# Performance work log

Measured on AMD Instinct MI355X. Metric: run time of the kernel, lower is better.

## Reference

```python
import jax, jax.numpy as jnp
import numpy as np

DN = ('NCHW', 'OIHW', 'NCHW')  # conv dimension numbers
EPS = 1e-5


def _tcn(x, w1, b1, w2, b2, w3, b3):
    """Gated TCN. x: [B,T,N,C] -> [B,T-2,N,Cout].  out = conv1(x)*sigmoid(conv2(x)) + tanh(conv3(x))"""
    xc = jnp.transpose(x, (0, 3, 2, 1))  # [B,C,N,T]
    conv = lambda w, b: jax.lax.conv_general_dilated(xc, w, (1, 1), 'VALID', dimension_numbers=DN) + b[None, :, None, None]
    p = conv(w1, b1)
    q = jax.nn.sigmoid(conv(w2, b2))
    r = jnp.tanh(conv(w3, b3))
    out = p * q + r  # [B,Cout,N,T-2]
    return jnp.transpose(out, (0, 3, 2, 1))


def setup_inputs() -> dict:
    key = jax.random.key(0)
    ks = jax.random.split(key, 16)
    B, T, N, C_in = 32, 24, 1024, 1
    K, C_t, C_s = 3, 64, 16
    inp = {}
    inp['x'] = jax.random.normal(ks[0], (B, T, N, C_in), jnp.float32)
    # stacked Chebyshev polynomials T_0..T_{K-1}, scaled so matmul output stays O(1)
    inp['cheb'] = jax.random.normal(ks[1], (K, N, N), jnp.float32) * (N ** -0.5)
    # temporal conv 1 (C_in -> C_t), kernel (1,3)
    s1 = (2.0 / (C_in * 3 + C_t * 3)) ** 0.5
    for i, nm in enumerate(['t1_w1', 't1_w2', 't1_w3']):
        inp[nm] = jax.random.normal(ks[2 + i], (C_t, C_in, 1, 3), jnp.float32) * s1
        inp[nm.replace('w', 'b')] = jnp.zeros((C_t,), jnp.float32)
    # Chebyshev weights (K, C_t, C_s), xavier-normal
    sc = (2.0 / (C_t + C_s)) ** 0.5
    inp['w_cheb'] = jax.random.normal(ks[5], (K, C_t, C_s), jnp.float32) * sc
    inp['b_cheb'] = jnp.zeros((C_s,), jnp.float32)
    # temporal conv 2 (C_s -> C_s)
    s2 = (2.0 / (C_s * 3 + C_s * 3)) ** 0.5
    for i, nm in enumerate(['t2_w1', 't2_w2', 't2_w3']):
        inp[nm] = jax.random.normal(ks[6 + i], (C_s, C_s, 1, 3), jnp.float32) * s2
        inp[nm.replace('w', 'b')] = jnp.zeros((C_s,), jnp.float32)
    # BatchNorm2d over num_nodes channel
    inp['bn_gamma'] = jnp.ones((N,), jnp.float32)
    inp['bn_beta'] = jnp.zeros((N,), jnp.float32)
    return inp


def reference(x, cheb, t1_w1, t1_b1, t1_w2, t1_b2, t1_w3, t1_b3,
              w_cheb, b_cheb, t2_w1, t2_b1, t2_w2, t2_b2, t2_w3, t2_b3,
              bn_gamma, bn_beta):
    # gated TCN 1: [B,24,N,1] -> [B,22,N,64]
    h = _tcn(x, t1_w1, t1_b1, t1_w2, t1_b2, t1_w3, t1_b3)
    # Chebyshev graph conv fused over all time steps and K taps:
    # T_k_x[b,t,n,c] = sum_m h[b,t,m,c] * cheb[k,m,n]; out = sum_k T_k_x @ W[k]
    s = jnp.einsum('btmc,kmn,kco->btno', h, cheb, w_cheb) + b_cheb  # [B,22,N,16]
    # gated TCN 2: -> [B,20,N,16]
    h2 = _tcn(s, t2_w1, t2_b1, t2_w2, t2_b2, t2_w3, t2_b3)
    # BatchNorm2d over node dim (training-mode batch stats), matching permute(0,2,1,3)
    y = jnp.transpose(h2, (0, 2, 1, 3))  # [B,N,T',C]
    mean = jnp.mean(y, axis=(0, 2, 3), keepdims=True)
    var = jnp.var(y, axis=(0, 2, 3), keepdims=True)  # biased, like torch BN
    y = (y - mean) * jax.lax.rsqrt(var + EPS) * bn_gamma[None, :, None, None] + bn_beta[None, :, None, None]
    y = jnp.transpose(y, (0, 2, 1, 3))  # [B,T',N,C]
    return jax.nn.relu(y)
```

## Files before the change

kernel.cpp:

```cpp
#include <hip/hip_runtime.h>
#include <hip/hip_bf16.h>

using bf16x8 = __attribute__((ext_vector_type(8))) short;
using bf16x4 = __attribute__((ext_vector_type(4))) short;
using f32x4  = __attribute__((ext_vector_type(4))) float;
using f32x2  = __attribute__((ext_vector_type(2))) float;

static __device__ __forceinline__ float bf2f(short s) {
  union { unsigned u; float f; } z;
  z.u = ((unsigned)(unsigned short)s) << 16;
  return z.f;
}
static __device__ __forceinline__ short f2bfs(float f) {
  union { __hip_bfloat16 h; short s; } u;
  u.h = __float2bfloat16(f);
  return u.s;
}
static __device__ __forceinline__ float frcp(float x) { return __builtin_amdgcn_rcpf(x); }
static __device__ __forceinline__ float sigm_f(float x) { return frcp(1.f + __expf(-x)); }
static __device__ __forceinline__ float tanh_f(float x) {
  return fmaf(2.f, frcp(1.f + __expf(-2.f * x)), -1.f);
}

typedef const __attribute__((address_space(1))) unsigned int* gas_u32;
typedef __attribute__((address_space(3))) unsigned int* las_u32;
#define GLOAD16(gp, lp) __builtin_amdgcn_global_load_lds( \
    (gas_u32)(const void*)(gp), (las_u32)(void*)(lp), 16, 0, 0)

__global__ void __launch_bounds__(256) k_transpose_cheb(
    const float* __restrict__ cheb, __hip_bfloat16* __restrict__ chebT,
    const float* __restrict__ wcheb, __hip_bfloat16* __restrict__ pbw) {
  int blk = blockIdx.x;
  if (blk == 768) {
    for (int i = threadIdx.x; i < 3072; i += 256) {
      int jj = i & 7, lane = (i >> 3) & 63, ksk = i >> 9;
      int kk = ksk >> 1, ks = ksk & 1;
      int c = ks * 32 + ((lane >> 4) & 3) * 8 + jj;
      int o = lane & 15;
      pbw[i] = __float2bfloat16(wcheb[kk * 1024 + c * 16 + o]);
    }
    return;
  }
  __shared__ float tile[64][65];
  int k = blk >> 8;
  int rem = blk & 255;
  int m0 = (rem >> 4) << 6;
  int n0 = (rem & 15) << 6;
  int tx = threadIdx.x & 63;
  int ty = threadIdx.x >> 6;
  const float* src = cheb + (size_t)k * 1024 * 1024;
  #pragma unroll
  for (int i = 0; i < 16; i++) {
    int ml = ty + i * 4;
    tile[ml][tx] = src[(size_t)(m0 + ml) * 1024 + n0 + tx];
  }
  __syncthreads();
  #pragma unroll
  for (int i = 0; i < 16; i++) {
    int nl = ty + i * 4;
    chebT[(size_t)(n0 + nl) * 3072 + k * 1024 + m0 + tx] =
        __float2bfloat16(tile[tx][nl]);
  }
}

__global__ void __launch_bounds__(256) k_tcn1_proj(
    const float* __restrict__ x,
    const float* __restrict__ w1, const float* __restrict__ b1,
    const float* __restrict__ w2, const float* __restrict__ b2,
    const float* __restrict__ w3, const float* __restrict__ b3,
    const __hip_bfloat16* __restrict__ pbw,
    __hip_bfloat16* __restrict__ hwt, int bt0) {
  __shared__ __align__(16) char hls[32768];
  const int tid = threadIdx.x;
  const int lane = tid & 63, w = tid >> 6;
  const int r16 = lane & 15, kb = lane >> 4;
  const int btl = blockIdx.x >> 2;
  const int m0 = (blockIdx.x & 3) << 8;
  const int bt = bt0 + btl;
  const int b = bt / 22, t = bt % 22;

  const float* xp = x + (size_t)(b * 24 + t) * 1024 + m0 + tid;
  const float x0 = xp[0], x1 = xp[1024], x2 = xp[2048];
  const f32x2 x0v = {x0, x0}, x1v = {x1, x1}, x2v = {x2, x2};

  bf16x8 bw[3][2];
  const bf16x8* pb8 = reinterpret_cast<const bf16x8*>(pbw);
  #pragma unroll
  for (int kk = 0; kk < 3; kk++)
    #pragma unroll
    for (int ks = 0; ks < 2; ks++)
      bw[kk][ks] = pb8[(kk * 2 + ks) * 64 + lane];

  const int rswz = (tid & 7) << 4;
  #pragma unroll
  for (int cg = 0; cg < 8; cg++) {
    bf16x8 hv;
    #pragma unroll
    for (int j2 = 0; j2 < 4; j2++) {
      const int c2 = cg * 4 + j2;
      const int wi = 6 * c2;
      f32x2 pw, qw, rw;
      pw = (f32x2){b1[2*c2], b1[2*c2+1]};
      qw = (f32x2){b2[2*c2], b2[2*c2+1]};
      rw = (f32x2){b3[2*c2], b3[2*c2+1]};
      pw = __builtin_elementwise_fma(x0v, (f32x2){w1[wi], w1[wi+3]}, pw);
      qw = __builtin_elementwise_fma(x0v, (f32x2){w2[wi], w2[wi+3]}, qw);
      rw = __builtin_elementwise_fma(x0v, (f32x2){w3[wi], w3[wi+3]}, rw);
      pw = __builtin_elementwise_fma(x1v, (f32x2){w1[wi+1], w1[wi+4]}, pw);
      qw = __builtin_elementwise_fma(x1v, (f32x2){w2[wi+1], w2[wi+4]}, qw);
      rw = __builtin_elementwise_fma(x1v, (f32x2){w3[wi+1], w3[wi+4]}, rw);
      pw = __builtin_elementwise_fma(x2v, (f32x2){w1[wi+2], w1[wi+5]}, pw);
      qw = __builtin_elementwise_fma(x2v, (f32x2){w2[wi+2], w2[wi+5]}, qw);
      rw = __builtin_elementwise_fma(x2v, (f32x2){w3[wi+2], w3[wi+5]}, rw);
      hv[j2*2+0] = f2bfs(fmaf(pw.x, sigm_f(qw.x), tanh_f(rw.x)));
      hv[j2*2+1] = f2bfs(fmaf(pw.y, sigm_f(qw.y), tanh_f(rw.y)));
    }
    *(bf16x8*)(hls + tid * 128 + ((cg << 4) ^ rswz)) = hv;
  }
  __syncthreads();

  const char* Ab = hls + (w * 64 + r16) * 128;
  const int axor = (r16 & 7) << 4;
  f32x4 acc[4][3];
  #pragma unroll
  for (int mt = 0; mt < 4; mt++)
    #pragma unroll
    for (int kk = 0; kk < 3; kk++) acc[mt][kk] = (f32x4){0.f, 0.f, 0.f, 0.f};

  #pragma unroll
  for (int ks = 0; ks < 2; ks++) {
    #pragma unroll
    for (int mt = 0; mt < 4; mt++) {
      bf16x8 a = *(const bf16x8*)(Ab + mt * 2048 + ((((ks << 2) + kb) << 4) ^ axor));
      #pragma unroll
      for (int kk = 0; kk < 3; kk++)
        acc[mt][kk] = __builtin_amdgcn_mfma_f32_16x16x32_bf16(a, bw[kk][ks], acc[mt][kk], 0, 0, 0);
    }
  }

  __hip_bfloat16* hp = hwt + (size_t)btl * 49152 + r16 * 3072 + m0 + w * 64;
  #pragma unroll
  for (int kk = 0; kk < 3; kk++)
    #pragma unroll
    for (int mt = 0; mt < 4; mt++) {
      bf16x4 v;
      #pragma unroll
      for (int r = 0; r < 4; r++) v[r] = f2bfs(acc[mt][kk][r]);
      *(bf16x4*)(hp + kk * 1024 + mt * 16 + kb * 4) = v;
    }
}

__global__ void __launch_bounds__(256, 2) k_gemm(
    const __hip_bfloat16* __restrict__ chebT,
    const __hip_bfloat16* __restrict__ hwt,
    const float* __restrict__ b_cheb,
    __hip_bfloat16* __restrict__ sbuf,
    int bt_base) {
  __shared__ __align__(16) char smem[32768];
  const int tid = threadIdx.x;
  const int lane = tid & 63;
  const int w = tid >> 6;

  int nt, ct;
  if (gridDim.x == 704) {
    const int xcd = blockIdx.x & 7;
    const int idx = blockIdx.x >> 3;
    nt = ((xcd >> 2) << 2) + (idx & 3);
    ct = (xcd & 3) * 22 + (idx >> 2);
  } else {
    nt = blockIdx.x & 7;
    ct = blockIdx.x >> 3;
  }

  const int srow = tid >> 3;
  const int sswz = ((tid & 7) ^ (srow & 7)) << 4;
  const char* Ag = (const char*)chebT + (size_t)(nt * 128 + srow) * 6144 + sswz;
  const int btl = srow >> 4, so = srow & 15;
  const char* Bg = (const char*)hwt + (size_t)(ct * 8 + btl) * 98304 + (size_t)so * 6144 + sswz;
  char* Als = smem + w * 1024;
  char* Bls = smem + 16384 + w * 1024;

  const int r16 = lane & 15;
  const int c16 = lane >> 4;
  const int wr = (w >> 1) << 6;
  const int wc = (w & 1) << 6;
  const int axor = (r16 & 7) << 4;
  const char* Abase = smem + (wr + r16) * 128;
  const char* Bbase = smem + 16384 + (wc + r16) * 128;

  f32x4 acc[4][4];
  #pragma unroll
  for (int i = 0; i < 4; i++)
    #pragma unroll
    for (int j = 0; j < 4; j++) acc[i][j] = (f32x4){0.f, 0.f, 0.f, 0.f};

  for (int kt = 0; kt < 48; kt++) {
    __syncthreads();
    const char* a = Ag + kt * 128;
    const char* b = Bg + kt * 128;
    #pragma unroll
    for (int i = 0; i < 4; i++) GLOAD16(a + i * 196608, Als + i * 4096);
    #pragma unroll
    for (int i = 0; i < 4; i++) GLOAD16(b + i * 196608, Bls + i * 4096);
    __syncthreads();
    #pragma unroll
    for (int ksub = 0; ksub < 2; ksub++) {
      const int ko = (ksub * 64 + c16 * 16) ^ axor;
      bf16x8 af[4], bfr[4];
      #pragma unroll
      for (int i = 0; i < 4; i++) af[i] = *(const bf16x8*)(Abase + i * 2048 + ko);
      #pragma unroll
      for (int j = 0; j < 4; j++) bfr[j] = *(const bf16x8*)(Bbase + j * 2048 + ko);
      #pragma unroll
      for (int i = 0; i < 4; i++)
        #pragma unroll
        for (int j = 0; j < 4; j++)
          acc[i][j] = __builtin_amdgcn_mfma_f32_16x16x32_bf16(af[i], bfr[j], acc[i][j], 0, 0, 0);
    }
  }

  float bias = b_cheb[r16];
  #pragma unroll
  for (int j = 0; j < 4; j++) {
    int gcol = ct * 128 + wc + j * 16 + r16;
    size_t bt_g = (size_t)bt_base + (gcol >> 4);
    int o = gcol & 15;
    #pragma unroll
    for (int i = 0; i < 4; i++) {
      int n0 = nt * 128 + wr + i * 16 + c16 * 4;
      __hip_bfloat16* sp = sbuf + (bt_g * 1024 + n0) * 16 + o;
      #pragma unroll
      for (int r = 0; r < 4; r++)
        sp[r * 16] = __float2bfloat16(acc[i][j][r] + bias);
    }
  }
}

__global__ void __launch_bounds__(256) k_tcn2(
    const __hip_bfloat16* __restrict__ sbuf,
    const float* __restrict__ w1, const float* __restrict__ b1,
    const float* __restrict__ w2, const float* __restrict__ b2,
    const float* __restrict__ w3, const float* __restrict__ b3,
    __hip_bfloat16* __restrict__ h2b) {
  const int tid = threadIdx.x;
  const int lane = tid & 63, w = tid >> 6;
  const int r16 = lane & 15, kb = lane >> 4;
  const int half = blockIdx.x & 1;
  const int bt2 = blockIdx.x >> 1;
  const int b = bt2 / 20, t2 = bt2 % 20;

  bf16x8 bw[3][2];
  const float* wps[3] = {w1, w2, w3};
  #pragma unroll
  for (int c = 0; c < 3; c++) {
    #pragma unroll
    for (int jj = 0; jj < 8; jj++) {
      int k = kb * 8 + jj;
      bw[c][0][jj] = f2bfs(wps[c][r16 * 48 + (k & 15) * 3 + (k >> 4)]);
      bw[c][1][jj] = (kb < 2) ? f2bfs(wps[c][r16 * 48 + (kb * 8 + jj) * 3 + 2]) : (short)0;
    }
  }
  const float bp = b1[r16], bq = b2[r16], br = b3[r16];

  const char* sb = (const char*)sbuf;
  const size_t slice = (size_t)1024 * 32;
  const int rowbase = half * 512 + w * 128;
  const char* baseA = sb + (size_t)(b * 22 + t2 + (kb >> 1)) * slice
                      + (size_t)(rowbase + r16) * 32 + (kb & 1) * 16;
  const char* baseC = sb + (size_t)(b * 22 + t2 + 2) * slice
                      + (size_t)(rowbase + r16) * 32 + (kb & 1) * 16;
  __hip_bfloat16* outp = h2b + ((size_t)bt2 * 1024 + rowbase + kb * 4) * 16 + r16;

  const f32x4 zro = {0.f, 0.f, 0.f, 0.f};
  #pragma unroll 2
  for (int i = 0; i < 8; i++) {
    bf16x8 a0 = *(const bf16x8*)(baseA + i * 512);
    bf16x8 a1{};
    if (kb < 2) a1 = *(const bf16x8*)(baseC + i * 512);
    f32x4 ap = __builtin_amdgcn_mfma_f32_16x16x32_bf16(a0, bw[0][0], zro, 0, 0, 0);
    f32x4 aq = __builtin_amdgcn_mfma_f32_16x16x32_bf16(a0, bw[1][0], zro, 0, 0, 0);
    f32x4 ar = __builtin_amdgcn_mfma_f32_16x16x32_bf16(a0, bw[2][0], zro, 0, 0, 0);
    ap = __builtin_amdgcn_mfma_f32_16x16x32_bf16(a1, bw[0][1], ap, 0, 0, 0);
    aq = __builtin_amdgcn_mfma_f32_16x16x32_bf16(a1, bw[1][1], aq, 0, 0, 0);
    ar = __builtin_amdgcn_mfma_f32_16x16x32_bf16(a1, bw[2][1], ar, 0, 0, 0);
    #pragma unroll
    for (int r = 0; r < 4; r++) {
      float h = fmaf(ap[r] + bp, sigm_f(aq[r] + bq), tanh_f(ar[r] + br));
      outp[(size_t)(i * 16 + r) * 16] = __float2bfloat16(h);
    }
  }
}

__global__ void __launch_bounds__(256) k_stats(
    const __hip_bfloat16* __restrict__ h2b, const float* __restrict__ gamma,
    const float* __restrict__ beta, float* __restrict__ ab) {
  int n = blockIdx.x;
  int tid = threadIdx.x;
  float s = 0.f, s2 = 0.f;
  int part = tid & 1;
  for (int bt2 = tid >> 1; bt2 < 640; bt2 += 128) {
    bf16x8 v = *(const bf16x8*)((const char*)h2b +
        ((size_t)bt2 * 1024 + n) * 32 + part * 16);
    #pragma unroll
    for (int j = 0; j < 8; j++) { float f = bf2f(v[j]); s += f; s2 += f * f; }
  }
  #pragma unroll
  for (int off = 32; off; off >>= 1) { s += __shfl_down(s, off); s2 += __shfl_down(s2, off); }
  __shared__ float rs[4], rs2[4];
  if ((tid & 63) == 0) { rs[tid >> 6] = s; rs2[tid >> 6] = s2; }
  __syncthreads();
  if (tid == 0) {
    float S = rs[0] + rs[1] + rs[2] + rs[3];
    float S2 = rs2[0] + rs2[1] + rs2[2] + rs2[3];
    float mean = S * (1.f / 10240.f);
    float var = S2 * (1.f / 10240.f) - mean * mean;
    float a = gamma[n] * rsqrtf(var + 1e-5f);
    ab[n] = a;
    ab[1024 + n] = beta[n] - mean * a;
  }
}

__global__ void __launch_bounds__(256) k_bnrelu(
    const __hip_bfloat16* __restrict__ h2b, const float* __restrict__ ab,
    float* __restrict__ out) {
  size_t c = (size_t)blockIdx.x * 256 + threadIdx.x;
  int n = (int)((c >> 1) & 1023);
  float a = ab[n], cc = ab[1024 + n];
  bf16x8 v = *(const bf16x8*)((const char*)h2b + c * 16);
  float4* op = reinterpret_cast<float4*>(out + c * 8);
  float4 o0, o1;
  o0.x = fmaxf(0.f, fmaf(bf2f(v[0]), a, cc));
  o0.y = fmaxf(0.f, fmaf(bf2f(v[1]), a, cc));
  o0.z = fmaxf(0.f, fmaf(bf2f(v[2]), a, cc));
  o0.w = fmaxf(0.f, fmaf(bf2f(v[3]), a, cc));
  o1.x = fmaxf(0.f, fmaf(bf2f(v[4]), a, cc));
  o1.y = fmaxf(0.f, fmaf(bf2f(v[5]), a, cc));
  o1.z = fmaxf(0.f, fmaf(bf2f(v[6]), a, cc));
  o1.w = fmaxf(0.f, fmaf(bf2f(v[7]), a, cc));
  op[0] = o0;
  op[1] = o1;
}

extern "C" void kernel_launch(void* const* d_in, const int* in_sizes, int n_in,
                              void* d_out, int out_size, void* d_ws, size_t ws_size,
                              hipStream_t stream) {
  const float* x     = (const float*)d_in[0];
  const float* cheb  = (const float*)d_in[1];
  const float* t1w1  = (const float*)d_in[2];
  const float* t1b1  = (const float*)d_in[3];
  const float* t1w2  = (const float*)d_in[4];
  const float* t1b2  = (const float*)d_in[5];
  const float* t1w3  = (const float*)d_in[6];
  const float* t1b3  = (const float*)d_in[7];
  const float* wch   = (const float*)d_in[8];
  const float* bch   = (const float*)d_in[9];
  const float* t2w1  = (const float*)d_in[10];
  const float* t2b1  = (const float*)d_in[11];
  const float* t2w2  = (const float*)d_in[12];
  const float* t2b2  = (const float*)d_in[13];
  const float* t2w3  = (const float*)d_in[14];
  const float* t2b3  = (const float*)d_in[15];
  const float* gam   = (const float*)d_in[16];
  const float* bet   = (const float*)d_in[17];

  char* ws = (char*)d_ws;
  __hip_bfloat16* chebT = (__hip_bfloat16*)ws;
  __hip_bfloat16* sbuf  = (__hip_bfloat16*)(ws + 6291456);
  float*          ab    = (float*)(ws + 29360128);
  __hip_bfloat16* pbw   = (__hip_bfloat16*)(ws + 29368320);
  __hip_bfloat16* h2b   = (__hip_bfloat16*)(ws + 29376512);
  __hip_bfloat16* hwt   = (__hip_bfloat16*)(ws + 50348032);

  size_t avail = ws_size > 50348032 ? ws_size - 50348032 : 0;
  int maxch = (int)(avail / 98304);
  maxch &= ~7;
  if (maxch > 704) maxch = 704;
  if (maxch < 8) maxch = 8;

  k_transpose_cheb<<<769, 256, 0, stream>>>(cheb, chebT, wch, pbw);

  for (int bt0 = 0; bt0 < 704; bt0 += maxch) {
    int ch = (704 - bt0 < maxch) ? (704 - bt0) : maxch;
    k_tcn1_proj<<<ch * 4, 256, 0, stream>>>(x, t1w1, t1b1, t1w2, t1b2, t1w3, t1b3,
                                            pbw, hwt, bt0);
    k_gemm<<<ch, 256, 0, stream>>>(chebT, hwt, bch, sbuf, bt0);
  }

  k_tcn2<<<1280, 256, 0, stream>>>(sbuf, t2w1, t2b1, t2w2, t2b2, t2w3, t2b3, h2b);
  k_stats<<<1024, 256, 0, stream>>>(h2b, gam, bet, ab);
  k_bnrelu<<<5120, 256, 0, stream>>>(h2b, ab, (float*)d_out);
}
```

Baseline: 180.0 us.

## Fuse cheb transpose into TCN1 launch and merge BN stats with normalize

After: 168.0 us, median of 2. 6.7% less time.

```diff
diff --git a/kernel.cpp b/kernel.cpp
--- a/kernel.cpp
+++ b/kernel.cpp
@@ -27,51 +27,43 @@
 #define GLOAD16(gp, lp) __builtin_amdgcn_global_load_lds( \
     (gas_u32)(const void*)(gp), (las_u32)(void*)(lp), 16, 0, 0)
 
-__global__ void __launch_bounds__(256) k_transpose_cheb(
-    const float* __restrict__ cheb, __hip_bfloat16* __restrict__ chebT,
-    const float* __restrict__ wcheb, __hip_bfloat16* __restrict__ pbw) {
-  int blk = blockIdx.x;
-  if (blk == 768) {
-    for (int i = threadIdx.x; i < 3072; i += 256) {
-      int jj = i & 7, lane = (i >> 3) & 63, ksk = i >> 9;
-      int kk = ksk >> 1, ks = ksk & 1;
-      int c = ks * 32 + ((lane >> 4) & 3) * 8 + jj;
-      int o = lane & 15;
-      pbw[i] = __float2bfloat16(wcheb[kk * 1024 + c * 16 + o]);
-    }
-    return;
-  }
-  __shared__ float tile[64][65];
-  int k = blk >> 8;
-  int rem = blk & 255;
-  int m0 = (rem >> 4) << 6;
-  int n0 = (rem & 15) << 6;
-  int tx = threadIdx.x & 63;
-  int ty = threadIdx.x >> 6;
-  const float* src = cheb + (size_t)k * 1024 * 1024;
-  #pragma unroll
-  for (int i = 0; i < 16; i++) {
-    int ml = ty + i * 4;
-    tile[ml][tx] = src[(size_t)(m0 + ml) * 1024 + n0 + tx];
-  }
-  __syncthreads();
-  #pragma unroll
-  for (int i = 0; i < 16; i++) {
-    int nl = ty + i * 4;
-    chebT[(size_t)(n0 + nl) * 3072 + k * 1024 + m0 + tx] =
-        __float2bfloat16(tile[tx][nl]);
-  }
-}
-
-__global__ void __launch_bounds__(256) k_tcn1_proj(
+__global__ void __launch_bounds__(256) k_front(
     const float* __restrict__ x,
     const float* __restrict__ w1, const float* __restrict__ b1,
     const float* __restrict__ w2, const float* __restrict__ b2,
     const float* __restrict__ w3, const float* __restrict__ b3,
-    const __hip_bfloat16* __restrict__ pbw,
-    __hip_bfloat16* __restrict__ hwt, int bt0) {
-  __shared__ __align__(16) char hls[32768];
+    const float* __restrict__ wcheb,
+    __hip_bfloat16* __restrict__ hwt, int bt0, int ch,
+    const float* __restrict__ cheb, __hip_bfloat16* __restrict__ chebT) {
+  __shared__ __align__(16) char smem[32768];
   const int tid = threadIdx.x;
+
+  if ((int)blockIdx.x >= ch * 4) {
+    float (*tile)[65] = reinterpret_cast<float (*)[65]>(smem);
+    int blk = blockIdx.x - ch * 4;
+    int k = blk >> 8;
+    int rem = blk & 255;
+    int m0 = (rem >> 4) << 6;
+    int n0 = (rem & 15) << 6;
+    int tx = tid & 63;
+    int ty = tid >> 6;
+    const float* src = cheb + (size_t)k * 1024 * 1024;
+    #pragma unroll
+    for (int i = 0; i < 16; i++) {
+      int ml = ty + i * 4;
+      tile[ml][tx] = src[(size_t)(m0 + ml) * 1024 + n0 + tx];
+    }
+    __syncthreads();
+    #pragma unroll
+    for (int i = 0; i < 16; i++) {
+      int nl = ty + i * 4;
+      chebT[(size_t)(n0 + nl) * 3072 + k * 1024 + m0 + tx] =
+          __float2bfloat16(tile[tx][nl]);
+    }
+    return;
+  }
+
+  char* hls = smem;
   const int lane = tid & 63, w = tid >> 6;
   const int r16 = lane & 15, kb = lane >> 4;
   const int btl = blockIdx.x >> 2;
@@ -84,12 +76,13 @@
   const f32x2 x0v = {x0, x0}, x1v = {x1, x1}, x2v = {x2, x2};
 
   bf16x8 bw[3][2];
-  const bf16x8* pb8 = reinterpret_cast<const bf16x8*>(pbw);
   #pragma unroll
   for (int kk = 0; kk < 3; kk++)
     #pragma unroll
     for (int ks = 0; ks < 2; ks++)
-      bw[kk][ks] = pb8[(kk * 2 + ks) * 64 + lane];
+      #pragma unroll
+      for (int jj = 0; jj < 8; jj++)
+        bw[kk][ks][jj] = f2bfs(wcheb[kk * 1024 + (ks * 32 + kb * 8 + jj) * 16 + r16]);
 
   const int rswz = (tid & 7) << 4;
   #pragma unroll
@@ -99,10 +92,9 @@
     for (int j2 = 0; j2 < 4; j2++) {
       const int c2 = cg * 4 + j2;
       const int wi = 6 * c2;
-      f32x2 pw, qw, rw;
-      pw = (f32x2){b1[2*c2], b1[2*c2+1]};
-      qw = (f32x2){b2[2*c2], b2[2*c2+1]};
-      rw = (f32x2){b3[2*c2], b3[2*c2+1]};
+      f32x2 pw = {b1[2*c2], b1[2*c2+1]};
+      f32x2 qw = {b2[2*c2], b2[2*c2+1]};
+      f32x2 rw = {b3[2*c2], b3[2*c2+1]};
       pw = __builtin_elementwise_fma(x0v, (f32x2){w1[wi], w1[wi+3]}, pw);
       qw = __builtin_elementwise_fma(x0v, (f32x2){w2[wi], w2[wi+3]}, qw);
       rw = __builtin_elementwise_fma(x0v, (f32x2){w3[wi], w3[wi+3]}, rw);
@@ -291,54 +283,48 @@
   }
 }
 
-__global__ void __launch_bounds__(256) k_stats(
+__global__ void __launch_bounds__(256) k_bnstats(
     const __hip_bfloat16* __restrict__ h2b, const float* __restrict__ gamma,
-    const float* __restrict__ beta, float* __restrict__ ab) {
-  int n = blockIdx.x;
-  int tid = threadIdx.x;
+    const float* __restrict__ beta, float* __restrict__ out) {
+  __shared__ __align__(16) short col[10240];
+  __shared__ float rs[4], rs2[4];
+  const int n = blockIdx.x;
+  const int tid = threadIdx.x;
+  const int part = tid & 1;
   float s = 0.f, s2 = 0.f;
-  int part = tid & 1;
   for (int bt2 = tid >> 1; bt2 < 640; bt2 += 128) {
     bf16x8 v = *(const bf16x8*)((const char*)h2b +
         ((size_t)bt2 * 1024 + n) * 32 + part * 16);
+    *(bf16x8*)((char*)col + bt2 * 32 + part * 16) = v;
     #pragma unroll
     for (int j = 0; j < 8; j++) { float f = bf2f(v[j]); s += f; s2 += f * f; }
   }
   #pragma unroll
   for (int off = 32; off; off >>= 1) { s += __shfl_down(s, off); s2 += __shfl_down(s2, off); }
-  __shared__ float rs[4], rs2[4];
   if ((tid & 63) == 0) { rs[tid >> 6] = s; rs2[tid >> 6] = s2; }
   __syncthreads();
-  if (tid == 0) {
-    float S = rs[0] + rs[1] + rs[2] + rs[3];
-    float S2 = rs2[0] + rs2[1] + rs2[2] + rs2[3];
-    float mean = S * (1.f / 10240.f);
-    float var = S2 * (1.f / 10240.f) - mean * mean;
-    float a = gamma[n] * rsqrtf(var + 1e-5f);
-    ab[n] = a;
-    ab[1024 + n] = beta[n] - mean * a;
-  }
-}
-
-__global__ void __launch_bounds__(256) k_bnrelu(
-    const __hip_bfloat16* __restrict__ h2b, const float* __restrict__ ab,
-    float* __restrict__ out) {
-  size_t c = (size_t)blockIdx.x * 256 + threadIdx.x;
-  int n = (int)((c >> 1) & 1023);
-  float a = ab[n], cc = ab[1024 + n];
-  bf16x8 v = *(const bf16x8*)((const char*)h2b + c * 16);
-  float4* op = reinterpret_cast<float4*>(out + c * 8);
-  float4 o0, o1;
-  o0.x = fmaxf(0.f, fmaf(bf2f(v[0]), a, cc));
-  o0.y = fmaxf(0.f, fmaf(bf2f(v[1]), a, cc));
-  o0.z = fmaxf(0.f, fmaf(bf2f(v[2]), a, cc));
-  o0.w = fmaxf(0.f, fmaf(bf2f(v[3]), a, cc));
-  o1.x = fmaxf(0.f, fmaf(bf2f(v[4]), a, cc));
-  o1.y = fmaxf(0.f, fmaf(bf2f(v[5]), a, cc));
-  o1.z = fmaxf(0.f, fmaf(bf2f(v[6]), a, cc));
-  o1.w = fmaxf(0.f, fmaf(bf2f(v[7]), a, cc));
-  op[0] = o0;
-  op[1] = o1;
+  const float S  = rs[0] + rs[1] + rs[2] + rs[3];
+  const float S2 = rs2[0] + rs2[1] + rs2[2] + rs2[3];
+  const float mean = S * (1.f / 10240.f);
+  const float var  = S2 * (1.f / 10240.f) - mean * mean;
+  const float a = gamma[n] * rsqrtf(var + 1e-5f);
+  const float c = beta[n] - mean * a;
+
+  for (int bt2 = tid >> 1; bt2 < 640; bt2 += 128) {
+    bf16x8 v = *(const bf16x8*)((const char*)col + bt2 * 32 + part * 16);
+    float4* op = reinterpret_cast<float4*>(out + ((size_t)bt2 * 1024 + n) * 16 + part * 8);
+    float4 o0, o1;
+    o0.x = fmaxf(0.f, fmaf(bf2f(v[0]), a, c));
+    o0.y = fmaxf(0.f, fmaf(bf2f(v[1]), a, c));
+    o0.z = fmaxf(0.f, fmaf(bf2f(v[2]), a, c));
+    o0.w = fmaxf(0.f, fmaf(bf2f(v[3]), a, c));
+    o1.x = fmaxf(0.f, fmaf(bf2f(v[4]), a, c));
+    o1.y = fmaxf(0.f, fmaf(bf2f(v[5]), a, c));
+    o1.z = fmaxf(0.f, fmaf(bf2f(v[6]), a, c));
+    o1.w = fmaxf(0.f, fmaf(bf2f(v[7]), a, c));
+    op[0] = o0;
+    op[1] = o1;
+  }
 }
 
 extern "C" void kernel_launch(void* const* d_in, const int* in_sizes, int n_in,
@@ -366,27 +352,25 @@
   char* ws = (char*)d_ws;
   __hip_bfloat16* chebT = (__hip_bfloat16*)ws;
   __hip_bfloat16* sbuf  = (__hip_bfloat16*)(ws + 6291456);
-  float*          ab    = (float*)(ws + 29360128);
-  __hip_bfloat16* pbw   = (__hip_bfloat16*)(ws + 29368320);
-  __hip_bfloat16* h2b   = (__hip_bfloat16*)(ws + 29376512);
-  __hip_bfloat16* hwt   = (__hip_bfloat16*)(ws + 50348032);
-
-  size_t avail = ws_size > 50348032 ? ws_size - 50348032 : 0;
+  __hip_bfloat16* h2b   = (__hip_bfloat16*)(ws + 29360128);
+  __hip_bfloat16* hwt   = (__hip_bfloat16*)(ws + 50331648);
+
+  size_t avail = ws_size > 50331648 ? ws_size - 50331648 : 0;
   int maxch = (int)(avail / 98304);
   maxch &= ~7;
   if (maxch > 704) maxch = 704;
   if (maxch < 8) maxch = 8;
 
-  k_transpose_cheb<<<769, 256, 0, stream>>>(cheb, chebT, wch, pbw);
-
+  int first = 1;
   for (int bt0 = 0; bt0 < 704; bt0 += maxch) {
     int ch = (704 - bt0 < maxch) ? (704 - bt0) : maxch;
-    k_tcn1_proj<<<ch * 4, 256, 0, stream>>>(x, t1w1, t1b1, t1w2, t1b2, t1w3, t1b3,
-                                            pbw, hwt, bt0);
+    int extra = first ? 768 : 0;
+    k_front<<<ch * 4 + extra, 256, 0, stream>>>(
+        x, t1w1, t1b1, t1w2, t1b2, t1w3, t1b3, wch, hwt, bt0, ch, cheb, chebT);
     k_gemm<<<ch, 256, 0, stream>>>(chebT, hwt, bch, sbuf, bt0);
+    first = 0;
   }
 
   k_tcn2<<<1280, 256, 0, stream>>>(sbuf, t2w1, t2b1, t2w2, t2b2, t2w3, t2b3, h2b);
-  k_stats<<<1024, 256, 0, stream>>>(h2b, gam, bet, ab);
-  k_bnrelu<<<5120, 256, 0, stream>>>(h2b, ab, (float*)d_out);
-}
+  k_bnstats<<<1024, 256, 0, stream>>>(h2b, gam, bet, (float*)d_out);
+}
```
